# Kernel optimization log

Measured on AMD Instinct MI355X. Metric: run time of the kernel, lower is better.

The kernel has to match this reference:

```python
import jax, jax.numpy as jnp
import numpy as np
from jax import lax

SCORE_THRESHOLD = 0.001
IOU_THRESHOLD = 0.7
MAX_DETECTIONS = 300
PRE_NMS_TOPK = 1024      # standard pre-NMS candidate cap (torchvision/YOLO practice)
CLASS_OFFSET = 4096.0    # > max image coord, separates classes so cross-class IoU == 0
IMG = 640.0

B, N, C = 32, 8400, 80


def setup_inputs() -> dict:
    key = jax.random.key(0)
    kc, ks, kp = jax.random.split(key, 3)
    # well-formed boxes in [y1, x1, y2, x2] convention (matches repo's nms())
    tl = jax.random.uniform(kc, (B, N, 2), jnp.float32, 0.0, IMG - 1.0)   # (y1, x1)
    wh = jax.random.uniform(ks, (B, N, 2), jnp.float32, 4.0, 160.0)      # (h, w)
    boxes = jnp.concatenate([tl, jnp.minimum(tl + wh, IMG)], axis=-1)     # [B,N,4]
    scores = jax.random.uniform(kp, (B, N, C), jnp.float32)               # [B,N,C]
    return {"boxes": boxes, "scores": scores}


def _pairwise_iou(b):
    # b: [B,K,4] as [y1,x1,y2,x2]; +1 pixel convention per the repo's nms()
    y1, x1, y2, x2 = b[..., 0], b[..., 1], b[..., 2], b[..., 3]
    areas = (x2 - x1 + 1.0) * (y2 - y1 + 1.0)                             # [B,K]
    yy1 = jnp.maximum(y1[:, :, None], y1[:, None, :])
    xx1 = jnp.maximum(x1[:, :, None], x1[:, None, :])
    yy2 = jnp.minimum(y2[:, :, None], y2[:, None, :])
    xx2 = jnp.minimum(x2[:, :, None], x2[:, None, :])
    w = jnp.maximum(0.0, xx2 - xx1 + 1.0)
    h = jnp.maximum(0.0, yy2 - yy1 + 1.0)
    inter = w * h                                                          # [B,K,K]
    return inter / (areas[:, :, None] + areas[:, None, :] - inter)


def multiclass_nms(boxes, scores):
    b, n, c = scores.shape
    flat = jnp.where(scores > SCORE_THRESHOLD, scores, 0.0).reshape(b, n * c)
    top_scores, top_idx = lax.top_k(flat, PRE_NMS_TOPK)                    # [B,K]
    box_idx = top_idx // c
    cls_idx = top_idx % c                                                  # int32 [B,K]
    cand = jnp.take_along_axis(boxes, box_idx[..., None], axis=1)          # [B,K,4]
    # offset boxes by class so per-class NMS happens in one shared pass
    off = cand + (cls_idx.astype(cand.dtype) * CLASS_OFFSET)[..., None]
    iou = _pairwise_iou(off)                                               # [B,K,K]

    k = PRE_NMS_TOPK
    idx = jnp.arange(k)
    keep0 = top_scores > SCORE_THRESHOLD                                   # [B,K]

    def body(i, keep):
        row = iou[:, i, :]                                                 # [B,K]
        sup = (row > IOU_THRESHOLD) & keep[:, i][:, None] & (idx[None, :] > i)
        return keep & ~sup

    keep = lax.fori_loop(0, k, body, keep0)                                # greedy NMS

    final_scores = jnp.where(keep, top_scores, 0.0)
    out_scores, sel = lax.top_k(final_scores, MAX_DETECTIONS)              # [B,300]
    out_boxes = jnp.take_along_axis(cand, sel[..., None], axis=1)          # [B,300,4]
    out_labels = jnp.take_along_axis(cls_idx, sel, axis=1)                 # [B,300]
    n_valid = jnp.minimum(jnp.sum(keep, axis=1, keepdims=True), MAX_DETECTIONS)
    return out_boxes, out_scores, out_labels.astype(jnp.int32), n_valid.astype(jnp.int32)


def reference(boxes, scores):
    return multiclass_nms(boxes, scores)
```

## Files before the change

kernel.cpp:

```cpp
#include <hip/hip_runtime.h>
#include <cstdint>
#include <cstddef>

#define B_      32
#define N_      8400
#define C_      80
#define NC      672000
#define NCV4    168000
#define NBINS   4096
#define TOPK    1024
#define MAXDET  300
#define CANDCAP 4096
#define NSLICE  16
#define SLICE_V4 10500
#define NBKT    8
#define SEGB    64
#define BSORT   256

#define STAGE_THRESH 0.998046875f

#define WS_SEGKEYS  0
#define WS_SEGCNT   2097152
#define WS_TOPSCORE 2113536
#define WS_TOPBOX   2244608
#define WS_CLSV     2768896
#define WS_KEEP     2801664

#define OUT_SCORES  38400
#define OUT_LABELS  48000
#define OUT_NVALID  57600

__global__ __launch_bounds__(256) void stage_kernel(const float4* __restrict__ scores4,
                                                    unsigned* __restrict__ segCnt,
                                                    unsigned long long* __restrict__ segKeys) {
    __shared__ unsigned lcnt[NBKT];
    int b = blockIdx.x, sl = blockIdx.y, tid = threadIdx.x;
    if (tid < NBKT) lcnt[tid] = 0;
    __syncthreads();
    const float4* s = scores4 + (size_t)b * NCV4 + (size_t)sl * SLICE_V4;
    for (int i = tid; i < SLICE_V4; i += 256) {
        float4 v = s[i];
        float c[4] = {v.x, v.y, v.z, v.w};
        unsigned flat0 = ((unsigned)sl * SLICE_V4 + (unsigned)i) * 4u;
        #pragma unroll
        for (int kc = 0; kc < 4; ++kc) {
            float x = (c[kc] > 0.001f) ? c[kc] : 0.0f;
            if (x >= STAGE_THRESH) {
                int bin = (int)(x * 4096.0f);
                bin = bin > (NBINS - 1) ? (NBINS - 1) : bin;
                int bkt = bin - 4088;
                unsigned p = atomicAdd(&lcnt[bkt], 1u);
                if (p < (unsigned)SEGB)
                    segKeys[(((size_t)(b * NBKT + bkt)) * NSLICE + sl) * SEGB + p] =
                        ((unsigned long long)__float_as_uint(x) << 32) |
                        (unsigned long long)(0xFFFFFFFFu - (flat0 + kc));
            }
        }
    }
    __syncthreads();
    if (tid < NBKT) segCnt[(b * NBKT + tid) * NSLICE + sl] = lcnt[tid];
}

__global__ __launch_bounds__(64) void select_kernel(
        const float4* __restrict__ scores4,
        const unsigned long long* __restrict__ segKeys,
        const unsigned* __restrict__ segCnt,
        const float4* __restrict__ boxes4,
        float* __restrict__ topScore,
        float4* __restrict__ topBox4,
        unsigned char* __restrict__ clsv,
        unsigned char* __restrict__ keepB) {
    __shared__ unsigned long long kbuf[CANDCAP];
    __shared__ unsigned scnt2[NBKT * NSLICE];
    __shared__ unsigned spref[NSLICE];
    __shared__ unsigned scnt;
    __shared__ int s_cut;
    int b = blockIdx.x, bkt = blockIdx.y, lane = threadIdx.x;

    scnt2[lane]      = segCnt[b * NBKT * NSLICE + lane];
    scnt2[lane + 64] = segCnt[b * NBKT * NSLICE + lane + 64];
    __threadfence_block();
    unsigned M = 0, base = 0, n = 0; int valid = 1;
    #pragma unroll
    for (int t = 0; t < NBKT; ++t) {
        unsigned s2 = 0, mx = 0;
        #pragma unroll
        for (int sl = 0; sl < NSLICE; ++sl) {
            unsigned v = scnt2[t * NSLICE + sl];
            s2 += v; mx = v > mx ? v : mx;
        }
        if (mx > (unsigned)SEGB || s2 > (unsigned)BSORT) valid = 0;
        M += s2;
        if (t > bkt) base += s2;
        if (t == bkt) n = s2;
    }
    if (M < (unsigned)TOPK || M > (unsigned)CANDCAP) valid = 0;

    if (valid) {
        if (bkt == 0) {
            uint4 z; z.x = 0u; z.y = 0u; z.z = 0u; z.w = 0u;
            ((uint4*)(keepB + (size_t)b * TOPK))[lane] = z;
        }
        if (base >= (unsigned)TOPK || n == 0) return;
        if (lane < NSLICE) {
            unsigned acc = 0;
            for (int s2 = 0; s2 < lane; ++s2) acc += scnt2[bkt * NSLICE + s2];
            spref[lane] = acc;
        }
        __threadfence_block();
        {
            int sl = lane & 15;
            int eo = lane >> 4;
            unsigned cA = scnt2[bkt * NSLICE + sl];
            unsigned b0 = spref[sl];
            const unsigned long long* src =
                segKeys + (((size_t)(b * NBKT + bkt)) * NSLICE + sl) * SEGB;
            for (int e = eo; e < (int)cA; e += 4) kbuf[b0 + e] = src[e];
            if (lane < 4) kbuf[n + lane] = 0ull;
        }
        __threadfence_block();
        int j0 = lane, j1 = lane + 64, j2 = lane + 128, j3 = lane + 192;
        unsigned long long k0 = (j0 < (int)n) ? kbuf[j0] : 0ull;
        unsigned long long k1 = (j1 < (int)n) ? kbuf[j1] : 0ull;
        unsigned long long k2 = (j2 < (int)n) ? kbuf[j2] : 0ull;
        unsigned long long k3 = (j3 < (int)n) ? kbuf[j3] : 0ull;
        unsigned r0 = 0, r1 = 0, r2 = 0, r3 = 0;
        for (unsigned i = 0; i < n; i += 4) {
            unsigned long long a = kbuf[i], b2 = kbuf[i + 1];
            unsigned long long c2 = kbuf[i + 2], d2 = kbuf[i + 3];
            r0 += (unsigned)(a > k0) + (unsigned)(b2 > k0) +
                  (unsigned)(c2 > k0) + (unsigned)(d2 > k0);
            r1 += (unsigned)(a > k1) + (unsigned)(b2 > k1) +
                  (unsigned)(c2 > k1) + (unsigned)(d2 > k1);
            r2 += (unsigned)(a > k2) + (unsigned)(b2 > k2) +
                  (unsigned)(c2 > k2) + (unsigned)(d2 > k2);
            r3 += (unsigned)(a > k3) + (unsigned)(b2 > k3) +
                  (unsigned)(c2 > k3) + (unsigned)(d2 > k3);
        }
        #pragma unroll
        for (int q = 0; q < 4; ++q) {
            int j = q == 0 ? j0 : q == 1 ? j1 : q == 2 ? j2 : j3;
            unsigned long long k = q == 0 ? k0 : q == 1 ? k1 : q == 2 ? k2 : k3;
            unsigned r = q == 0 ? r0 : q == 1 ? r1 : q == 2 ? r2 : r3;
            if (j < (int)n) {
                unsigned pos = base + r;
                if (pos < (unsigned)TOPK) {
                    float sc = __uint_as_float((unsigned)(k >> 32));
                    unsigned idx = 0xFFFFFFFFu - (unsigned)(k & 0xFFFFFFFFull);
                    if (idx >= (unsigned)NC) idx = 0;
                    unsigned bi = idx / (unsigned)C_;
                    unsigned cl = idx - bi * (unsigned)C_;
                    topScore[b * TOPK + pos] = sc;
                    topBox4[b * TOPK + pos] = boxes4[(size_t)b * N_ + bi];
                    clsv[(size_t)b * TOPK + pos] = (unsigned char)(0x80u | cl);
                }
            }
        }
        return;
    }

    if (bkt != 0) return;
    {
        uint4 z; z.x = 0u; z.y = 0u; z.z = 0u; z.w = 0u;
        ((uint4*)(keepB + (size_t)b * TOPK))[lane] = z;
    }
    unsigned* fh = (unsigned*)kbuf;
    for (int i2 = lane; i2 < NBINS; i2 += 64) fh[i2] = 0;
    if (lane == 0) scnt = 0;
    __threadfence_block();
    const float4* s = scores4 + (size_t)b * NCV4;
    for (int i2 = lane; i2 < NCV4; i2 += 64) {
        float4 v = s[i2];
        float c4[4] = {v.x, v.y, v.z, v.w};
        #pragma unroll
        for (int kc = 0; kc < 4; ++kc) {
            float x = (c4[kc] > 0.001f) ? c4[kc] : 0.0f;
            int bin = (int)(x * 4096.0f);
            bin = bin > (NBINS - 1) ? (NBINS - 1) : bin;
            atomicAdd(&fh[bin], 1u);
        }
    }
    __threadfence_block();
    if (lane == 0) {
        unsigned acc = 0; int cb = 0;
        for (int bin = NBINS - 1; bin >= 0; --bin) {
            acc += fh[bin];
            if (acc >= (unsigned)TOPK) { cb = bin; break; }
        }
        s_cut = cb;
    }
    __threadfence_block();
    int cb = s_cut;
    for (int i2 = lane; i2 < NCV4; i2 += 64) {
        float4 v = s[i2];
        float c4[4] = {v.x, v.y, v.z, v.w};
        unsigned flat0 = (unsigned)i2 * 4u;
        #pragma unroll
        for (int kc = 0; kc < 4; ++kc) {
            float x = (c4[kc] > 0.001f) ? c4[kc] : 0.0f;
            int bin = (int)(x * 4096.0f);
            bin = bin > (NBINS - 1) ? (NBINS - 1) : bin;
            if (bin >= cb) {
                unsigned p = atomicAdd(&scnt, 1u);
                if (p < (unsigned)CANDCAP)
                    kbuf[p] = ((unsigned long long)__float_as_uint(x) << 32) |
                              (unsigned long long)(0xFFFFFFFFu - (flat0 + kc));
            }
        }
    }
    __threadfence_block();
    unsigned M2 = scnt; if (M2 > (unsigned)CANDCAP) M2 = CANDCAP;
    int S = (M2 <= 1024u) ? 1024 : (M2 <= 2048u ? 2048 : CANDCAP);
    for (int i2 = (int)M2 + lane; i2 < S; i2 += 64) kbuf[i2] = 0ull;
    __threadfence_block();
    for (int kk = 2; kk <= S; kk <<= 1) {
        for (int j = kk >> 1; j > 0; j >>= 1) {
            for (int t = lane; t < S; t += 64) {
                int l = t ^ j;
                if (l > t) {
                    unsigned long long a0 = kbuf[t], c0 = kbuf[l];
                    bool sw = ((t & kk) == 0) ? (a0 < c0) : (a0 > c0);
                    if (sw) { kbuf[t] = c0; kbuf[l] = a0; }
                }
            }
            __threadfence_block();
        }
    }
    for (int r = lane; r < TOPK; r += 64) {
        unsigned long long key = kbuf[r];
        float sc = __uint_as_float((unsigned)(key >> 32));
        unsigned idx = 0xFFFFFFFFu - (unsigned)(key & 0xFFFFFFFFull);
        if (idx >= (unsigned)NC) idx = 0;
        unsigned bi = idx / (unsigned)C_;
        unsigned cl = idx - bi * (unsigned)C_;
        topScore[b * TOPK + r] = sc;
        topBox4[b * TOPK + r] = boxes4[(size_t)b * N_ + bi];
        clsv[(size_t)b * TOPK + r] =
            (unsigned char)((sc > 0.001f ? 0x80u : 0u) | cl);
    }
}

#define CLS_CAP 256
__global__ __launch_bounds__(64) void nms_kernel(const unsigned char* __restrict__ clsv,
                                                 const float4* __restrict__ topBox4,
                                                 unsigned char* __restrict__ keepB) {
    __shared__ unsigned short spos[CLS_CAP];
    __shared__ float by1[CLS_CAP], bx1[CLS_CAP], by2[CLS_CAP], bx2[CLS_CAP];
    __shared__ float barea[CLS_CAP];
    __shared__ unsigned char sup[CLS_CAP];
    int b = blockIdx.x;
    int c = blockIdx.y;
    int lane = threadIdx.x;
    unsigned char* kp = keepB + (size_t)b * TOPK;

    uint4 w = ((const uint4*)(clsv + (size_t)b * TOPK))[lane];
    unsigned target = 0x80u | (unsigned)c;
    unsigned mmask = 0; int cnt = 0;
    #pragma unroll
    for (int t = 0; t < 16; ++t) {
        unsigned d = (t < 4) ? w.x : (t < 8) ? w.y : (t < 12) ? w.z : w.w;
        unsigned v = (d >> ((t & 3) * 8)) & 0xffu;
        if (v == target) { mmask |= (1u << t); ++cnt; }
    }
    int x = cnt;
    #pragma unroll
    for (int o = 1; o < 64; o <<= 1) {
        int y = __shfl_up(x, o, 64);
        if (lane >= o) x += y;
    }
    int pre = x - cnt;
    int m = __shfl(x, 63, 64);
    int slot = pre;
    #pragma unroll
    for (int t = 0; t < 16; ++t) {
        if ((mmask >> t) & 1u) {
            if (slot < CLS_CAP) spos[slot] = (unsigned short)(lane * 16 + t);
            ++slot;
        }
    }
    int m2 = m < CLS_CAP ? m : CLS_CAP;
    __threadfence_block();
    float off = (float)c * 4096.0f;
    for (int j = lane; j < m2; j += 64) {
        int p = spos[j];
        float4 tb = topBox4[(size_t)b * TOPK + p];
        float y1 = tb.x + off, x1 = tb.y + off;
        float y2 = tb.z + off, x2 = tb.w + off;
        by1[j] = y1; bx1[j] = x1; by2[j] = y2; bx2[j] = x2;
        barea[j] = __fmul_rn((x2 - x1) + 1.0f, (y2 - y1) + 1.0f);
        sup[j] = 0;
    }
    __threadfence_block();
    int cur = 0;
    while (cur < m2) {
        if (lane == 0) kp[spos[cur]] = 1;
        float cy1 = by1[cur], cx1 = bx1[cur], cy2 = by2[cur], cx2 = bx2[cur];
        float carea = barea[cur];
        for (int j = cur + 1 + lane; j < m2; j += 64) {
            if (!sup[j]) {
                float yy1 = fmaxf(cy1, by1[j]), xx1 = fmaxf(cx1, bx1[j]);
                float yy2 = fminf(cy2, by2[j]), xx2 = fminf(cx2, bx2[j]);
                float w2 = fmaxf(0.0f, (xx2 - xx1) + 1.0f);
                float h2 = fmaxf(0.0f, (yy2 - yy1) + 1.0f);
                float inter = __fmul_rn(w2, h2);
                float denom = (carea + barea[j]) - inter;
                float iou = inter / denom;
                if (iou > 0.7f) sup[j] = 1;
            }
        }
        __threadfence_block();
        int nxt = m2;
        for (int j = cur + 1 + lane; j < m2; j += 64)
            if (!sup[j]) { nxt = j; break; }
        for (int o = 32; o > 0; o >>= 1) {
            int other = __shfl_xor(nxt, o, 64);
            nxt = nxt < other ? nxt : other;
        }
        cur = nxt;
    }
}

__global__ __launch_bounds__(1024) void finalize_kernel(const float* __restrict__ topScore,
                                                        const float4* __restrict__ topBox4,
                                                        const unsigned char* __restrict__ clsv,
                                                        const unsigned char* __restrict__ keepB,
                                                        float* __restrict__ out) {
    __shared__ int wsum[16];
    __shared__ int sel[MAXDET];
    int b = blockIdx.x;
    int tid = threadIdx.x;
    int lane = tid & 63;
    int wave = tid >> 6;
    int kp = keepB[(size_t)b * TOPK + tid];
    unsigned long long mb = __ballot(kp != 0);
    int wpre = __popcll(mb & ((1ull << lane) - 1ull));
    if (lane == 0) wsum[wave] = __popcll(mb);
    __syncthreads();
    int wbase = 0, nk = 0;
    #pragma unroll
    for (int t = 0; t < 16; ++t) {
        int v = wsum[t];
        if (t < wave) wbase += v;
        nk += v;
    }
    int kexcl = wbase + wpre;
    int sexcl = tid - kexcl;
    if (kp) {
        if (kexcl < MAXDET) sel[kexcl] = tid;
    } else {
        int slot = nk + sexcl;
        if (slot < MAXDET) sel[slot] = tid;
    }
    __syncthreads();
    if (tid < MAXDET) {
        int p = sel[tid];
        float sc = (tid < nk) ? topScore[b * TOPK + p] : 0.0f;
        float4 tb = topBox4[(size_t)b * TOPK + p];
        float* ob = out + ((size_t)b * MAXDET + tid) * 4;
        ob[0] = tb.x; ob[1] = tb.y; ob[2] = tb.z; ob[3] = tb.w;
        out[OUT_SCORES + b * MAXDET + tid] = sc;
        out[OUT_LABELS + b * MAXDET + tid] =
            (float)(clsv[(size_t)b * TOPK + p] & 0x7f);
    }
    if (tid == 0) out[OUT_NVALID + b] = (float)(nk < MAXDET ? nk : MAXDET);
}

extern "C" void kernel_launch(void* const* d_in, const int* in_sizes, int n_in,
                              void* d_out, int out_size, void* d_ws, size_t ws_size,
                              hipStream_t stream) {
    const float* boxes  = (const float*)d_in[0];
    const float* scores = (const float*)d_in[1];
    float* out = (float*)d_out;
    char* ws = (char*)d_ws;

    unsigned long long* segKeys = (unsigned long long*)(ws + WS_SEGKEYS);
    unsigned* segCnt = (unsigned*)(ws + WS_SEGCNT);
    float* topScore = (float*)(ws + WS_TOPSCORE);
    float4* topBox4 = (float4*)(ws + WS_TOPBOX);
    unsigned char* clsv = (unsigned char*)(ws + WS_CLSV);
    unsigned char* keepB = (unsigned char*)(ws + WS_KEEP);

    const float4* scores4 = (const float4*)scores;
    const float4* boxes4  = (const float4*)boxes;

    stage_kernel<<<dim3(B_, NSLICE), 256, 0, stream>>>(scores4, segCnt, segKeys);
    select_kernel<<<dim3(B_, NBKT), 64, 0, stream>>>(scores4, segKeys, segCnt, boxes4,
                                                     topScore, topBox4, clsv, keepB);
    nms_kernel<<<dim3(B_, C_), 64, 0, stream>>>(clsv, topBox4, keepB);
    finalize_kernel<<<B_, 1024, 0, stream>>>(topScore, topBox4, clsv, keepB, out);
}
```

Before: 174.2 us.

## Pack four classes per NMS block and stage candidate boxes in shared memory

The NMS kernel now runs four waves per block, each handling one class, and first loads the batch's 1024 candidate boxes and class bytes cooperatively into shared memory. Each per-class wave then gathers its boxes from LDS instead of issuing scattered global loads. This cuts redundant global reads and the launch block count by four, at the cost of more shared memory per block and a block barrier. The select kernel's segment-count load is also vectorised to uint2.

```diff
diff --git a/kernel.cpp b/kernel.cpp
--- a/kernel.cpp
+++ b/kernel.cpp
@@ -77,8 +77,11 @@
     __shared__ int s_cut;
     int b = blockIdx.x, bkt = blockIdx.y, lane = threadIdx.x;
 
-    scnt2[lane]      = segCnt[b * NBKT * NSLICE + lane];
-    scnt2[lane + 64] = segCnt[b * NBKT * NSLICE + lane + 64];
+    {
+        uint2 cc = ((const uint2*)(segCnt + b * NBKT * NSLICE))[lane];
+        scnt2[lane * 2]     = cc.x;
+        scnt2[lane * 2 + 1] = cc.y;
+    }
     __threadfence_block();
     unsigned M = 0, base = 0, n = 0; int valid = 1;
     #pragma unroll
@@ -241,24 +244,35 @@
 }
 
 #define CLS_CAP 256
-__global__ __launch_bounds__(64) void nms_kernel(const unsigned char* __restrict__ clsv,
-                                                 const float4* __restrict__ topBox4,
-                                                 unsigned char* __restrict__ keepB) {
-    __shared__ unsigned short spos[CLS_CAP];
-    __shared__ float by1[CLS_CAP], bx1[CLS_CAP], by2[CLS_CAP], bx2[CLS_CAP];
-    __shared__ float barea[CLS_CAP];
-    __shared__ unsigned char sup[CLS_CAP];
-    int b = blockIdx.x;
-    int c = blockIdx.y;
-    int lane = threadIdx.x;
+#define NMS_CPB 4
+__global__ __launch_bounds__(256) void nms_kernel(const unsigned char* __restrict__ clsv,
+                                                  const float4* __restrict__ topBox4,
+                                                  unsigned char* __restrict__ keepB) {
+    __shared__ float4 sBox[TOPK];
+    __shared__ unsigned sClsv[TOPK / 4];
+    __shared__ unsigned short spos[NMS_CPB][CLS_CAP];
+    __shared__ float by1[NMS_CPB][CLS_CAP], bx1[NMS_CPB][CLS_CAP];
+    __shared__ float by2[NMS_CPB][CLS_CAP], bx2[NMS_CPB][CLS_CAP];
+    __shared__ float barea[NMS_CPB][CLS_CAP];
+    __shared__ unsigned char sup[NMS_CPB][CLS_CAP];
+    int b = blockIdx.x, g = blockIdx.y, tid = threadIdx.x;
+    int lane = tid & 63, wave = tid >> 6;
     unsigned char* kp = keepB + (size_t)b * TOPK;
 
-    uint4 w = ((const uint4*)(clsv + (size_t)b * TOPK))[lane];
+    sClsv[tid] = ((const unsigned*)(clsv + (size_t)b * TOPK))[tid];
+    #pragma unroll
+    for (int r = 0; r < 4; ++r)
+        sBox[r * 256 + tid] = topBox4[(size_t)b * TOPK + r * 256 + tid];
+    __syncthreads();
+
+    int c = g * NMS_CPB + wave;
+    unsigned d0 = sClsv[lane * 4 + 0], d1 = sClsv[lane * 4 + 1];
+    unsigned d2 = sClsv[lane * 4 + 2], d3 = sClsv[lane * 4 + 3];
     unsigned target = 0x80u | (unsigned)c;
     unsigned mmask = 0; int cnt = 0;
     #pragma unroll
     for (int t = 0; t < 16; ++t) {
-        unsigned d = (t < 4) ? w.x : (t < 8) ? w.y : (t < 12) ? w.z : w.w;
+        unsigned d = (t < 4) ? d0 : (t < 8) ? d1 : (t < 12) ? d2 : d3;
         unsigned v = (d >> ((t & 3) * 8)) & 0xffu;
         if (v == target) { mmask |= (1u << t); ++cnt; }
     }
@@ -274,7 +288,7 @@
     #pragma unroll
     for (int t = 0; t < 16; ++t) {
         if ((mmask >> t) & 1u) {
-            if (slot < CLS_CAP) spos[slot] = (unsigned short)(lane * 16 + t);
+            if (slot < CLS_CAP) spos[wave][slot] = (unsigned short)(lane * 16 + t);
             ++slot;
         }
     }
@@ -282,36 +296,37 @@
     __threadfence_block();
     float off = (float)c * 4096.0f;
     for (int j = lane; j < m2; j += 64) {
-        int p = spos[j];
-        float4 tb = topBox4[(size_t)b * TOPK + p];
+        int p = spos[wave][j];
+        float4 tb = sBox[p];
         float y1 = tb.x + off, x1 = tb.y + off;
         float y2 = tb.z + off, x2 = tb.w + off;
-        by1[j] = y1; bx1[j] = x1; by2[j] = y2; bx2[j] = x2;
-        barea[j] = __fmul_rn((x2 - x1) + 1.0f, (y2 - y1) + 1.0f);
-        sup[j] = 0;
+        by1[wave][j] = y1; bx1[wave][j] = x1; by2[wave][j] = y2; bx2[wave][j] = x2;
+        barea[wave][j] = __fmul_rn((x2 - x1) + 1.0f, (y2 - y1) + 1.0f);
+        sup[wave][j] = 0;
     }
     __threadfence_block();
     int cur = 0;
     while (cur < m2) {
-        if (lane == 0) kp[spos[cur]] = 1;
-        float cy1 = by1[cur], cx1 = bx1[cur], cy2 = by2[cur], cx2 = bx2[cur];
-        float carea = barea[cur];
+        if (lane == 0) kp[spos[wave][cur]] = 1;
+        float cy1 = by1[wave][cur], cx1 = bx1[wave][cur];
+        float cy2 = by2[wave][cur], cx2 = bx2[wave][cur];
+        float carea = barea[wave][cur];
         for (int j = cur + 1 + lane; j < m2; j += 64) {
-            if (!sup[j]) {
-                float yy1 = fmaxf(cy1, by1[j]), xx1 = fmaxf(cx1, bx1[j]);
-                float yy2 = fminf(cy2, by2[j]), xx2 = fminf(cx2, bx2[j]);
+            if (!sup[wave][j]) {
+                float yy1 = fmaxf(cy1, by1[wave][j]), xx1 = fmaxf(cx1, bx1[wave][j]);
+                float yy2 = fminf(cy2, by2[wave][j]), xx2 = fminf(cx2, bx2[wave][j]);
                 float w2 = fmaxf(0.0f, (xx2 - xx1) + 1.0f);
                 float h2 = fmaxf(0.0f, (yy2 - yy1) + 1.0f);
                 float inter = __fmul_rn(w2, h2);
-                float denom = (carea + barea[j]) - inter;
+                float denom = (carea + barea[wave][j]) - inter;
                 float iou = inter / denom;
-                if (iou > 0.7f) sup[j] = 1;
+                if (iou > 0.7f) sup[wave][j] = 1;
             }
         }
         __threadfence_block();
         int nxt = m2;
         for (int j = cur + 1 + lane; j < m2; j += 64)
-            if (!sup[j]) { nxt = j; break; }
+            if (!sup[wave][j]) { nxt = j; break; }
         for (int o = 32; o > 0; o >>= 1) {
             int other = __shfl_xor(nxt, o, 64);
             nxt = nxt < other ? nxt : other;
@@ -386,6 +401,6 @@
     stage_kernel<<<dim3(B_, NSLICE), 256, 0, stream>>>(scores4, segCnt, segKeys);
     select_kernel<<<dim3(B_, NBKT), 64, 0, stream>>>(scores4, segKeys, segCnt, boxes4,
                                                      topScore, topBox4, clsv, keepB);
-    nms_kernel<<<dim3(B_, C_), 64, 0, stream>>>(clsv, topBox4, keepB);
+    nms_kernel<<<dim3(B_, C_ / NMS_CPB), 256, 0, stream>>>(clsv, topBox4, keepB);
     finalize_kernel<<<B_, 1024, 0, stream>>>(topScore, topBox4, clsv, keepB, out);
 }
```

New measurement: 175.2 us. About the same (+0.5%).
